# Kernel optimization log

Hardware: AMD Instinct MI355X
Metric: run time of the kernel (lower is better)

## Reference

```python
import jax, jax.numpy as jnp
import numpy as np


def _conv(x, k, pad):
    # x: NHWC, k: HWIO
    return jax.lax.conv_general_dilated(x, k, (1, 1), pad,
                                        dimension_numbers=('NHWC', 'HWIO', 'NHWC'))


def _hard_sigmoid(z):
    return jnp.clip(0.2 * z + 0.5, 0.0, 1.0)


def _convlstm(x_seq, Wx, Wh, b, return_sequences):
    # x_seq: (B,T,H,W,C); Wx: (5,5,C,4F) VALID; Wh: (5,5,F,4F) SAME; b: (4F,)
    B, T, H, W, C = x_seq.shape
    F4 = Wx.shape[-1]
    F = F4 // 4
    # input-to-state convs for all timesteps in one batched conv
    xz = _conv(x_seq.reshape(B * T, H, W, C), Wx, 'VALID') + b
    Ho, Wo = xz.shape[1], xz.shape[2]
    xz = xz.reshape(B, T, Ho, Wo, F4).transpose(1, 0, 2, 3, 4)  # time-major
    h0 = jnp.zeros((B, Ho, Wo, F), x_seq.dtype)
    c0 = h0

    def step(carry, xt):
        h, c = carry
        z = xt + _conv(h, Wh, 'SAME')
        zi, zf, zc, zo = jnp.split(z, 4, axis=-1)  # keras gate order i,f,c,o
        i = _hard_sigmoid(zi)
        f = _hard_sigmoid(zf)
        o = _hard_sigmoid(zo)
        c = f * c + i * jnp.tanh(zc)
        h = o * jnp.tanh(c)
        return (h, c), (h if return_sequences else None)

    (h, c), hs = jax.lax.scan(step, (h0, c0), xz)
    if return_sequences:
        return hs.transpose(1, 0, 2, 3, 4)  # back to (B,T,Ho,Wo,F)
    return h


def setup_inputs() -> dict:
    key = jax.random.key(0)
    ks = jax.random.split(key, 12)
    B, T, H, W, C = 16, 6, 64, 64, 5

    def p(k, shape, scale=0.05):
        return jax.random.normal(k, shape, dtype=jnp.float32) * scale

    x = jax.random.normal(ks[0], (B, T, H, W, C), dtype=jnp.float32)
    # layer1: Cin=5 -> F=128
    Wx1 = p(ks[1], (5, 5, 5, 512));   Wh1 = p(ks[2], (5, 5, 128, 512));  b1 = jnp.zeros((512,), jnp.float32)
    # layer2: Cin=128 -> F=64
    Wx2 = p(ks[3], (5, 5, 128, 256)); Wh2 = p(ks[4], (5, 5, 64, 256));   b2 = jnp.zeros((256,), jnp.float32)
    # layer3: Cin=64 -> F=64
    Wx3 = p(ks[5], (5, 5, 64, 256));  Wh3 = p(ks[6], (5, 5, 64, 256));   b3 = jnp.zeros((256,), jnp.float32)
    D = 52 * 52 * 64  # 173056 after three valid 5x5 convs
    Wd1 = p(ks[7], (D, 1024), 0.01);  bd1 = jnp.zeros((1024,), jnp.float32)
    Wd2 = p(ks[8], (1024, 1024));     bd2 = jnp.zeros((1024,), jnp.float32)
    Wd3 = p(ks[9], (1024, 4));        bd3 = jnp.zeros((4,), jnp.float32)
    return dict(x=x, Wx1=Wx1, Wh1=Wh1, b1=b1, Wx2=Wx2, Wh2=Wh2, b2=b2,
                Wx3=Wx3, Wh3=Wh3, b3=b3, Wd1=Wd1, bd1=bd1, Wd2=Wd2, bd2=bd2,
                Wd3=Wd3, bd3=bd3)


def reference(x, Wx1, Wh1, b1, Wx2, Wh2, b2, Wx3, Wh3, b3,
              Wd1, bd1, Wd2, bd2, Wd3, bd3):
    # NOTE: the original call() computes an average-pool of the input but then
    # overwrites it with conv1(inputs); the pooled branch is dead code.
    h = _convlstm(x, Wx1, Wh1, b1, True)   # (B,T,60,60,128)
    h = _convlstm(h, Wx2, Wh2, b2, True)   # (B,T,56,56,64)
    h = _convlstm(h, Wx3, Wh3, b3, False)  # (B,52,52,64)
    z = h.reshape(h.shape[0], -1)          # keras Flatten = row-major H,W,C
    z = jax.nn.relu(z @ Wd1 + bd1)
    z = jax.nn.relu(z @ Wd2 + bd2)
    return z @ Wd3 + bd3                   # (B,4)
```

## Files before the change

### kernel.cpp

```cpp
#include <hip/hip_runtime.h>

typedef __bf16 bf16;
typedef bf16 bf16x8 __attribute__((ext_vector_type(8)));
typedef float f32x4 __attribute__((ext_vector_type(4)));

__device__ inline bf16x8 bzero8() {
  bf16x8 v;
#pragma unroll
  for (int i = 0; i < 8; ++i) v[i] = (bf16)0.f;
  return v;
}

__device__ __forceinline__ void gload_lds16(const bf16* g, bf16* l) {
  __builtin_amdgcn_global_load_lds(
      (const __attribute__((address_space(1))) void*)g,
      (__attribute__((address_space(3))) void*)l, 16, 0, 0);
}

template <int CIN, int LOG2C>
__global__ void __launch_bounds__(256)
conv_gemm128(const bf16* __restrict__ in, const bf16* __restrict__ wt,
             const float* __restrict__ bias, const bf16* __restrict__ xz,
             bf16* __restrict__ out_bf, float* __restrict__ out_f,
             int HoWo, int Wo, int inH, int inW,
             int T, int t, int N, int K, int epi)
{
  __shared__ bf16 As[128 * 32];
  __shared__ bf16 Bs[128 * 32];

  const int tid  = threadIdx.x;
  const int w    = tid >> 6;
  const int lane = tid & 63;
  const int n0 = blockIdx.x * 128;
  const int m0 = blockIdx.y * 128;

  const int srow = w * 16 + (lane >> 2);
  const int kq   = lane & 3;
  const long inHW = (long)inH * inW;

  long base_a[2];
#pragma unroll
  for (int j = 0; j < 2; ++j) {
    const int am  = m0 + srow + j * 64;
    const int img = am / HoWo;
    const int p   = am - img * HoWo;
    const int ay  = p / Wo;
    const int ax  = p - ay * Wo;
    base_a[j] = (img * inHW + (long)ay * inW + ax) << LOG2C;
  }
  const bf16* wrow0 = wt + (long)(n0 + srow) * K;
  const bf16* wrow1 = wt + (long)(n0 + srow + 64) * K;

  f32x4 acc[4][4];
#pragma unroll
  for (int r = 0; r < 4; ++r)
#pragma unroll
    for (int cq = 0; cq < 4; ++cq) {
      acc[r][cq][0] = 0.f; acc[r][cq][1] = 0.f;
      acc[r][cq][2] = 0.f; acc[r][cq][3] = 0.f;
    }

  const int lrow = lane & 15;
  const int lq   = lane >> 4;
  const int wm   = w & 1;
  const int wn   = w >> 1;
  bf16* AsW = As + w * 512;
  bf16* BsW = Bs + w * 512;

#pragma unroll 4
  for (int k0 = 0; k0 < K; k0 += 32) {
    const int k  = k0 + kq * 8;
    const int c  = k & (CIN - 1);
    const int kc = k >> LOG2C;
    const int ky = kc / 5;
    const int kx = kc - ky * 5;
    const long off = ((long)(ky * inW + kx) << LOG2C) + c;
    gload_lds16(in + base_a[0] + off, AsW);
    gload_lds16(in + base_a[1] + off, AsW + 2048);
    gload_lds16(wrow0 + k, BsW);
    gload_lds16(wrow1 + k, BsW + 2048);
    __syncthreads();

    bf16x8 a_frag[4], b_frag[4];
#pragma unroll
    for (int r = 0; r < 4; ++r)
      a_frag[r] = *(const bf16x8*)&As[(wm * 64 + r * 16 + lrow) * 32 + lq * 8];
#pragma unroll
    for (int cq = 0; cq < 4; ++cq)
      b_frag[cq] = *(const bf16x8*)&Bs[(wn * 64 + cq * 16 + lrow) * 32 + lq * 8];
#pragma unroll
    for (int r = 0; r < 4; ++r)
#pragma unroll
      for (int cq = 0; cq < 4; ++cq)
        acc[r][cq] = __builtin_amdgcn_mfma_f32_16x16x32_bf16(a_frag[r], b_frag[cq],
                                                             acc[r][cq], 0, 0, 0);
    __syncthreads();
  }

  const int colb = n0 + wn * 64 + lrow;
  if (epi == 0) {
    float bsv[4];
#pragma unroll
    for (int cq = 0; cq < 4; ++cq) bsv[cq] = bias[colb + cq * 16];
#pragma unroll
    for (int r = 0; r < 4; ++r)
#pragma unroll
      for (int q = 0; q < 4; ++q) {
        const long row = m0 + wm * 64 + r * 16 + lq * 4 + q;
#pragma unroll
        for (int cq = 0; cq < 4; ++cq)
          out_bf[row * N + colb + cq * 16] = (bf16)(acc[r][cq][q] + bsv[cq]);
      }
  } else {
#pragma unroll
    for (int r = 0; r < 4; ++r)
#pragma unroll
      for (int q = 0; q < 4; ++q) {
        const int row = m0 + wm * 64 + r * 16 + lq * 4 + q;
        const int b   = row / HoWo;
        const int p   = row - b * HoWo;
        const long xrow = (long)(b * T + t) * HoWo + p;
#pragma unroll
        for (int cq = 0; cq < 4; ++cq) {
          const int nn = colb + cq * 16;
          out_f[(long)row * N + nn] = acc[r][cq][q] + (float)xz[xrow * N + nn];
        }
      }
  }
}

template <int CIN>
__global__ void __launch_bounds__(256)
conv_gemm64(const bf16* __restrict__ in, const bf16* __restrict__ wt,
            const float* __restrict__ bias, bf16* __restrict__ out_bf,
            int HoWo, int Wo, int inH, int inW, int N, int K)
{
  __shared__ bf16 As[64 * 40];
  __shared__ bf16 Bs[64 * 40];

  const int tid  = threadIdx.x;
  const int wave = tid >> 6;
  const int lane = tid & 63;
  const int m0 = blockIdx.x * 64;
  const int n0 = blockIdx.y * 64;

  const int srow = tid >> 2;
  const int skq  = tid & 3;

  const int am  = m0 + srow;
  const int ab  = am / HoWo;
  const int apx = am - ab * HoWo;
  const int ay  = apx / Wo;
  const int ax  = apx - ay * Wo;
  const long inHW = (long)inH * inW;
  const bf16* inb  = in + (long)ab * inHW * CIN;
  const bf16* wrow = wt + (long)(n0 + srow) * K;

  f32x4 acc[4];
#pragma unroll
  for (int r = 0; r < 4; ++r) { acc[r][0] = 0.f; acc[r][1] = 0.f; acc[r][2] = 0.f; acc[r][3] = 0.f; }

  const int lrow = lane & 15;
  const int lq   = lane >> 4;
  const int ksteps = (K + 31) >> 5;

  for (int ks = 0; ks < ksteps; ++ks) {
    const int k = (ks << 5) + skq * 8;
    bf16x8 av = bzero8(), bv = bzero8();
#pragma unroll
    for (int j = 0; j < 8; ++j) {
      const int ke = k + j;
      if (ke < K) {
        const int c  = ke % CIN;
        const int kc = ke / CIN;
        const int ky = kc / 5;
        const int kx = kc - ky * 5;
        const int iy = ay + ky;
        const int ix = ax + kx;
        av[j] = inb[((long)iy * inW + ix) * CIN + c];
        bv[j] = wrow[ke];
      }
    }
    *(bf16x8*)&As[srow * 40 + skq * 8] = av;
    *(bf16x8*)&Bs[srow * 40 + skq * 8] = bv;
    __syncthreads();

    bf16x8 bfrag = *(const bf16x8*)&Bs[(wave * 16 + lrow) * 40 + lq * 8];
#pragma unroll
    for (int r = 0; r < 4; ++r) {
      bf16x8 afrag = *(const bf16x8*)&As[(r * 16 + lrow) * 40 + lq * 8];
      acc[r] = __builtin_amdgcn_mfma_f32_16x16x32_bf16(afrag, bfrag, acc[r], 0, 0, 0);
    }
    __syncthreads();
  }

  const int col = n0 + wave * 16 + lrow;
  const float bsv = bias[col];
#pragma unroll
  for (int r = 0; r < 4; ++r)
#pragma unroll
    for (int q = 0; q < 4; ++q) {
      const long row = m0 + r * 16 + lq * 4 + q;
      out_bf[row * N + col] = (bf16)(acc[r][q] + bsv);
    }
}

__global__ void __launch_bounds__(256)
gate_kernel(const bf16* __restrict__ xz, const float* __restrict__ hz,
            float* __restrict__ c, bf16* __restrict__ hseq,
            bf16* __restrict__ hpad, float* __restrict__ hf,
            int HoWo, int Wo, int Wp, int HpWp, int F, int t, int T, int total)
{
  const int idx = blockIdx.x * 256 + threadIdx.x;
  if (idx >= total) return;
  const int f  = idx % F;
  const int bp = idx / F;
  const int b  = bp / HoWo;
  const int p  = bp - b * HoWo;
  const int N4 = 4 * F;

  float zi, zf, zc, zo;
  if (hz != nullptr) {
    const float* zp = hz + (long)bp * N4 + f;
    zi = zp[0]; zf = zp[F]; zc = zp[2 * F]; zo = zp[3 * F];
  } else {
    const bf16* zp = xz + ((long)(b * T + t) * HoWo + p) * N4 + f;
    zi = (float)zp[0]; zf = (float)zp[F]; zc = (float)zp[2 * F]; zo = (float)zp[3 * F];
  }
  const float cprev = (t > 0) ? c[idx] : 0.f;
  const float ig = fminf(fmaxf(0.2f * zi + 0.5f, 0.f), 1.f);
  const float fg = fminf(fmaxf(0.2f * zf + 0.5f, 0.f), 1.f);
  const float og = fminf(fmaxf(0.2f * zo + 0.5f, 0.f), 1.f);
  const float cn = fg * cprev + ig * tanhf(zc);
  const float h  = og * tanhf(cn);
  c[idx] = cn;
  const bf16 hb = (bf16)h;
  if (hseq != nullptr)
    hseq[((long)(b * T + t) * HoWo + p) * F + f] = hb;
  if (hpad != nullptr) {
    const int y = p / Wo;
    const int x = p - y * Wo;
    hpad[((long)b * HpWp + (long)(y + 2) * Wp + (x + 2)) * F + f] = hb;
  }
  if (hf != nullptr) hf[idx] = h;
}

__global__ void __launch_bounds__(256)
cast_f32_bf16(const float* __restrict__ in, bf16* __restrict__ out, int n)
{
  const int i = blockIdx.x * 256 + threadIdx.x;
  if (i < n) out[i] = (bf16)in[i];
}

__global__ void __launch_bounds__(256)
cast_transpose(const float* __restrict__ in, bf16* __restrict__ out, int K, int N)
{
  const int i = blockIdx.x * 256 + threadIdx.x;
  if (i < K * N) {
    const int k = i / N;
    const int n = i - k * N;
    out[(long)n * K + k] = (bf16)in[i];
  }
}

__global__ void __launch_bounds__(256)
dense_splitk(const float* __restrict__ A, const float* __restrict__ W,
             float* __restrict__ out, int D, int N, int chunk)
{
  const int j  = blockIdx.x * 256 + threadIdx.x;
  const int d0 = blockIdx.y * chunk;
  int d1 = d0 + chunk; if (d1 > D) d1 = D;
  float acc[16];
#pragma unroll
  for (int b = 0; b < 16; ++b) acc[b] = 0.f;
  for (int d = d0; d < d1; ++d) {
    const float w = W[(long)d * N + j];
#pragma unroll
    for (int b = 0; b < 16; ++b) acc[b] += A[(long)b * D + d] * w;
  }
#pragma unroll
  for (int b = 0; b < 16; ++b) atomicAdd(&out[b * N + j], acc[b]);
}

__global__ void __launch_bounds__(256)
bias_relu(const float* __restrict__ in, const float* __restrict__ bias,
          float* __restrict__ out, int N, int total)
{
  const int i = blockIdx.x * 256 + threadIdx.x;
  if (i < total) {
    const int j = i % N;
    const float v = in[i] + bias[j];
    out[i] = v > 0.f ? v : 0.f;
  }
}

__global__ void __launch_bounds__(256)
dense3_kernel(const float* __restrict__ z, const float* __restrict__ W,
              const float* __restrict__ bias, float* __restrict__ out)
{
  const int b = blockIdx.x;
  const int tid = threadIdx.x;
  float a0 = 0.f, a1 = 0.f, a2 = 0.f, a3 = 0.f;
  for (int d = tid; d < 1024; d += 256) {
    const float zv = z[b * 1024 + d];
    a0 += zv * W[d * 4 + 0]; a1 += zv * W[d * 4 + 1];
    a2 += zv * W[d * 4 + 2]; a3 += zv * W[d * 4 + 3];
  }
  __shared__ float red[256][4];
  red[tid][0] = a0; red[tid][1] = a1; red[tid][2] = a2; red[tid][3] = a3;
  __syncthreads();
  for (int s = 128; s > 0; s >>= 1) {
    if (tid < s) {
      red[tid][0] += red[tid + s][0]; red[tid][1] += red[tid + s][1];
      red[tid][2] += red[tid + s][2]; red[tid][3] += red[tid + s][3];
    }
    __syncthreads();
  }
  if (tid < 4) out[b * 4 + tid] = red[0][tid] + bias[tid];
}

extern "C" void kernel_launch(void* const* d_in, const int* in_sizes, int n_in,
                              void* d_out, int out_size, void* d_ws, size_t ws_size,
                              hipStream_t stream)
{
  const float* x   = (const float*)d_in[0];
  const float* Wx1 = (const float*)d_in[1];
  const float* Wh1 = (const float*)d_in[2];
  const float* b1  = (const float*)d_in[3];
  const float* Wx2 = (const float*)d_in[4];
  const float* Wh2 = (const float*)d_in[5];
  const float* b2  = (const float*)d_in[6];
  const float* Wx3 = (const float*)d_in[7];
  const float* Wh3 = (const float*)d_in[8];
  const float* b3  = (const float*)d_in[9];
  const float* Wd1 = (const float*)d_in[10];
  const float* bd1 = (const float*)d_in[11];
  const float* Wd2 = (const float*)d_in[12];
  const float* bd2 = (const float*)d_in[13];
  const float* Wd3 = (const float*)d_in[14];
  const float* bd3 = (const float*)d_in[15];

  char* ws = (char*)d_ws;
  size_t off = 0;
  auto alloc = [&](size_t bytes) -> void* {
    void* p = ws + off;
    off += (bytes + 255) & ~(size_t)255;
    return p;
  };
  bf16* x_bf = (bf16*)alloc((size_t)1966080 * 2);
  bf16* wx1t = (bf16*)alloc((size_t)64000 * 2);
  bf16* wh1t = (bf16*)alloc((size_t)1638400 * 2);
  bf16* wx2t = (bf16*)alloc((size_t)819200 * 2);
  bf16* wh2t = (bf16*)alloc((size_t)409600 * 2);
  bf16* wx3t = (bf16*)alloc((size_t)409600 * 2);
  bf16* wh3t = (bf16*)alloc((size_t)409600 * 2);
  bf16* xzA  = (bf16*)alloc((size_t)176947200 * 2);
  bf16* hB   = (bf16*)alloc((size_t)44236800 * 2);
  float* hzC = (float*)alloc((size_t)29491200 * 4);
  float* cA  = (float*)alloc((size_t)7372800 * 4);
  float* h3f = (float*)alloc((size_t)2768896 * 4);
  bf16* hpadA = (bf16*)alloc((size_t)8388608 * 2);
  float* out1 = (float*)alloc(16384 * 4);
  float* z1   = (float*)alloc(16384 * 4);
  float* out2 = (float*)alloc(16384 * 4);
  float* z2   = (float*)alloc(16384 * 4);

  bf16* h1seq = hB;
  bf16* h2seq = hB;
  float* c1 = cA;
  float* c2 = cA;
  float* c3 = cA + (size_t)3211264;
  bf16* hpad1 = hpadA;
  bf16* hpad2 = hpadA;
  bf16* hpad3 = hpadA + (size_t)3686400;

  cast_f32_bf16<<<(1966080 + 255) / 256, 256, 0, stream>>>(x, x_bf, 1966080);
  cast_transpose<<<(64000 + 255) / 256, 256, 0, stream>>>(Wx1, wx1t, 125, 512);
  cast_transpose<<<(1638400 + 255) / 256, 256, 0, stream>>>(Wh1, wh1t, 3200, 512);
  cast_transpose<<<(819200 + 255) / 256, 256, 0, stream>>>(Wx2, wx2t, 3200, 256);
  cast_transpose<<<(409600 + 255) / 256, 256, 0, stream>>>(Wh2, wh2t, 1600, 256);
  cast_transpose<<<(409600 + 255) / 256, 256, 0, stream>>>(Wx3, wx3t, 1600, 256);
  cast_transpose<<<(409600 + 255) / 256, 256, 0, stream>>>(Wh3, wh3t, 1600, 256);

  hipMemsetAsync(hpadA, 0, (size_t)8388608 * 2, stream);
  conv_gemm64<5><<<dim3(5400, 8), 256, 0, stream>>>(
      x_bf, wx1t, b1, xzA, 3600, 60, 64, 64, 512, 125);
  for (int t = 0; t < 6; ++t) {
    if (t > 0)
      conv_gemm128<128, 7><<<dim3(4, 450), 256, 0, stream>>>(
          hpad1, wh1t, nullptr, xzA, nullptr, hzC,
          3600, 60, 64, 64, 6, t, 512, 3200, 1);
    gate_kernel<<<28800, 256, 0, stream>>>(
        xzA, (t > 0) ? hzC : nullptr, c1, h1seq,
        (t < 5) ? hpad1 : nullptr, nullptr,
        3600, 60, 64, 4096, 128, t, 6, 7372800);
  }

  bf16* xz2 = xzA;
  conv_gemm128<128, 7><<<dim3(2, 2352), 256, 0, stream>>>(
      h1seq, wx2t, b2, nullptr, xz2, nullptr,
      3136, 56, 60, 60, 6, 0, 256, 3200, 0);
  hipMemsetAsync(hpad2, 0, (size_t)3686400 * 2, stream);
  for (int t = 0; t < 6; ++t) {
    if (t > 0)
      conv_gemm128<64, 6><<<dim3(2, 392), 256, 0, stream>>>(
          hpad2, wh2t, nullptr, xz2, nullptr, hzC,
          3136, 56, 60, 60, 6, t, 256, 1600, 1);
    gate_kernel<<<12544, 256, 0, stream>>>(
        xz2, (t > 0) ? hzC : nullptr, c2, h2seq,
        (t < 5) ? hpad2 : nullptr, nullptr,
        3136, 56, 60, 3600, 64, t, 6, 3211264);
  }

  bf16* xz3 = xzA;
  conv_gemm128<64, 6><<<dim3(2, 2028), 256, 0, stream>>>(
      h2seq, wx3t, b3, nullptr, xz3, nullptr,
      2704, 52, 56, 56, 6, 0, 256, 1600, 0);
  hipMemsetAsync(hpad3, 0, (size_t)3211264 * 2, stream);
  for (int t = 0; t < 6; ++t) {
    if (t > 0)
      conv_gemm128<64, 6><<<dim3(2, 338), 256, 0, stream>>>(
          hpad3, wh3t, nullptr, xz3, nullptr, hzC,
          2704, 52, 56, 56, 6, t, 256, 1600, 1);
    gate_kernel<<<10816, 256, 0, stream>>>(
        xz3, (t > 0) ? hzC : nullptr, c3, nullptr,
        (t < 5) ? hpad3 : nullptr, (t == 5) ? h3f : nullptr,
        2704, 52, 56, 3136, 64, t, 6, 2768896);
  }

  hipMemsetAsync(out1, 0, 16384 * 4, stream);
  hipMemsetAsync(out2, 0, 16384 * 4, stream);
  dense_splitk<<<dim3(4, 169), 256, 0, stream>>>(h3f, Wd1, out1, 173056, 1024, 1024);
  bias_relu<<<64, 256, 0, stream>>>(out1, bd1, z1, 1024, 16384);
  dense_splitk<<<dim3(4, 4), 256, 0, stream>>>(z1, Wd2, out2, 1024, 1024, 256);
  bias_relu<<<64, 256, 0, stream>>>(out2, bd2, z2, 1024, 16384);
  dense3_kernel<<<16, 256, 0, stream>>>(z2, Wd3, bd3, (float*)d_out);
}
```

Baseline: 5.428 ms.

## Rewrite implicit-GEMM conv as 256x256 double-buffered pipelined MFMA kernel

Replaces the 128x128 single-buffered conv GEMM with a 256x256-tile, 512-thread kernel that uses K=64 steps. It double-buffers LDS and interleaves async global-to-LDS loads for the next tile with MFMA quadrants, using raw barriers, vmcnt waits and setprio. It also XOR-swizzles the LDS layout to avoid bank conflicts and remaps workgroups across XCDs for L2 locality. The aim is to hide load latency and raise arithmetic intensity. The cost is higher register and LDS use, and fewer blocks for the small recurrent convs (e.g. 169-225 blocks), which may underfill the GPU.

```diff
diff --git a/kernel.cpp b/kernel.cpp
--- a/kernel.cpp
+++ b/kernel.cpp
@@ -17,113 +17,220 @@
       (__attribute__((address_space(3))) void*)l, 16, 0, 0);
 }
 
+#define MFMA16 __builtin_amdgcn_mfma_f32_16x16x32_bf16
+#define LGKM0 asm volatile("s_waitcnt lgkmcnt(0)")
+#define VMC2 asm volatile("s_waitcnt vmcnt(2)")
+#define VMC0 asm volatile("s_waitcnt vmcnt(0)")
+
 template <int CIN, int LOG2C>
-__global__ void __launch_bounds__(256)
-conv_gemm128(const bf16* __restrict__ in, const bf16* __restrict__ wt,
+__global__ void __launch_bounds__(512, 2)
+conv_gemm256(const bf16* __restrict__ in, const bf16* __restrict__ wt,
              const float* __restrict__ bias, const bf16* __restrict__ xz,
              bf16* __restrict__ out_bf, float* __restrict__ out_f,
              int HoWo, int Wo, int inH, int inW,
              int T, int t, int N, int K, int epi)
 {
-  __shared__ bf16 As[128 * 32];
-  __shared__ bf16 Bs[128 * 32];
+  __shared__ bf16 As[2][2][8192];
+  __shared__ bf16 Bs[2][2][8192];
 
   const int tid  = threadIdx.x;
   const int w    = tid >> 6;
   const int lane = tid & 63;
-  const int n0 = blockIdx.x * 128;
-  const int m0 = blockIdx.y * 128;
-
-  const int srow = w * 16 + (lane >> 2);
-  const int kq   = lane & 3;
+
+  const int gx  = gridDim.x;
+  const int nwg = gx * gridDim.y;
+  int flat = blockIdx.y * gx + blockIdx.x;
+  {
+    const int xcd = flat & 7, o = flat >> 3;
+    const int qq = nwg >> 3, rr = nwg & 7;
+    flat = (xcd < rr ? xcd * (qq + 1) : rr * (qq + 1) + (xcd - rr) * qq) + o;
+  }
+  const int n0 = (flat % gx) << 8;
+  const int m0 = (flat / gx) << 8;
+
   const long inHW = (long)inH * inW;
-
-  long base_a[2];
-#pragma unroll
-  for (int j = 0; j < 2; ++j) {
-    const int am  = m0 + srow + j * 64;
-    const int img = am / HoWo;
-    const int p   = am - img * HoWo;
-    const int ay  = p / Wo;
-    const int ax  = p - ay * Wo;
-    base_a[j] = (img * inHW + (long)ay * inW + ax) << LOG2C;
-  }
-  const bf16* wrow0 = wt + (long)(n0 + srow) * K;
-  const bf16* wrow1 = wt + (long)(n0 + srow + 64) * K;
-
-  f32x4 acc[4][4];
-#pragma unroll
-  for (int r = 0; r < 4; ++r)
-#pragma unroll
-    for (int cq = 0; cq < 4; ++cq) {
-      acc[r][cq][0] = 0.f; acc[r][cq][1] = 0.f;
-      acc[r][cq][2] = 0.f; acc[r][cq][3] = 0.f;
-    }
+  const int lr8  = lane >> 3;
+  const int koff = ((lane & 7) ^ lr8) << 3;
+
+  long baseA[2][2];
+  const bf16* wrowp[2][2];
+#pragma unroll
+  for (int h = 0; h < 2; ++h)
+#pragma unroll
+    for (int j = 0; j < 2; ++j) {
+      const int row = ((j * 8 + w) << 3) + lr8;
+      const int gm  = m0 + h * 128 + row;
+      const int img = gm / HoWo;
+      const int p   = gm - img * HoWo;
+      const int ay  = p / Wo;
+      const int ax  = p - ay * Wo;
+      baseA[h][j] = ((long)img * inHW + (long)ay * inW + ax) << LOG2C;
+      wrowp[h][j] = wt + (long)(n0 + h * 128 + row) * K + koff;
+    }
+
+  const int KT = K >> 6;
+
+  auto stage = [&](int kt, int half) {
+    if (kt >= KT) return;
+    const int slot = kt & 1;
+    if (half < 2) {
+      const int kk = kt << 6;
+      const int kc = kk >> LOG2C;
+      const int ky = kc / 5;
+      const int kx = kc - ky * 5;
+      const long toff = ((long)(ky * inW + kx) << LOG2C) + (kk & (CIN - 1)) + koff;
+      bf16* d = &As[slot][half][w << 9];
+      gload_lds16(in + baseA[half][0] + toff, d);
+      gload_lds16(in + baseA[half][1] + toff, d + 4096);
+    } else {
+      const int h = half - 2;
+      bf16* d = &Bs[slot][h][w << 9];
+      gload_lds16(wrowp[h][0] + (kt << 6), d);
+      gload_lds16(wrowp[h][1] + (kt << 6), d + 4096);
+    }
+  };
 
   const int lrow = lane & 15;
   const int lq   = lane >> 4;
-  const int wm   = w & 1;
-  const int wn   = w >> 1;
-  bf16* AsW = As + w * 512;
-  bf16* BsW = Bs + w * 512;
-
-#pragma unroll 4
-  for (int k0 = 0; k0 < K; k0 += 32) {
-    const int k  = k0 + kq * 8;
-    const int c  = k & (CIN - 1);
-    const int kc = k >> LOG2C;
-    const int ky = kc / 5;
-    const int kx = kc - ky * 5;
-    const long off = ((long)(ky * inW + kx) << LOG2C) + c;
-    gload_lds16(in + base_a[0] + off, AsW);
-    gload_lds16(in + base_a[1] + off, AsW + 2048);
-    gload_lds16(wrow0 + k, BsW);
-    gload_lds16(wrow1 + k, BsW + 2048);
-    __syncthreads();
-
-    bf16x8 a_frag[4], b_frag[4];
-#pragma unroll
-    for (int r = 0; r < 4; ++r)
-      a_frag[r] = *(const bf16x8*)&As[(wm * 64 + r * 16 + lrow) * 32 + lq * 8];
-#pragma unroll
-    for (int cq = 0; cq < 4; ++cq)
-      b_frag[cq] = *(const bf16x8*)&Bs[(wn * 64 + cq * 16 + lrow) * 32 + lq * 8];
-#pragma unroll
-    for (int r = 0; r < 4; ++r)
-#pragma unroll
-      for (int cq = 0; cq < 4; ++cq)
-        acc[r][cq] = __builtin_amdgcn_mfma_f32_16x16x32_bf16(a_frag[r], b_frag[cq],
-                                                             acc[r][cq], 0, 0, 0);
-    __syncthreads();
-  }
+  const int wm   = w >> 2;
+  const int wn   = w & 3;
+  const int s7   = lrow & 7;
+
+  auto rdA = [&](int slot, int r, int ks) -> bf16x8 {
+    const int row = (r << 4) + lrow;
+    const int ch  = ((ks << 2) + lq) ^ s7;
+    return *(const bf16x8*)&As[slot][wm][(row << 6) + (ch << 3)];
+  };
+  auto rdB = [&](int slot, int cq, int ks) -> bf16x8 {
+    const int row = ((wn & 1) << 6) + (cq << 4) + lrow;
+    const int ch  = ((ks << 2) + lq) ^ s7;
+    return *(const bf16x8*)&Bs[slot][wn >> 1][(row << 6) + (ch << 3)];
+  };
+
+  f32x4 acc[8][4];
+#pragma unroll
+  for (int r = 0; r < 8; ++r)
+#pragma unroll
+    for (int c = 0; c < 4; ++c) {
+      acc[r][c][0] = 0.f; acc[r][c][1] = 0.f;
+      acc[r][c][2] = 0.f; acc[r][c][3] = 0.f;
+    }
+
+#define QUAD(RB, CB)                                                          \
+  __builtin_amdgcn_s_setprio(1);                                              \
+  _Pragma("unroll")                                                           \
+  for (int r = 0; r < 4; ++r)                                                 \
+    _Pragma("unroll")                                                         \
+    for (int c = 0; c < 2; ++c) {                                             \
+      acc[RB + r][CB + c] =                                                   \
+          MFMA16(af[r][0], bq[CB + c][0], acc[RB + r][CB + c], 0, 0, 0);      \
+      acc[RB + r][CB + c] =                                                   \
+          MFMA16(af[r][1], bq[CB + c][1], acc[RB + r][CB + c], 0, 0, 0);      \
+    }                                                                         \
+  __builtin_amdgcn_s_setprio(0);
+
+  stage(0, 0); stage(0, 1); stage(0, 2); stage(0, 3);
+  stage(1, 0);
+  VMC2;
+  __builtin_amdgcn_s_barrier();
+
+  bf16x8 af[4][2], bq[4][2];
+  const int NI = KT >> 1;
+  for (int i = 0; i < NI; ++i) {
+    const int t1 = 2 * i + 1, t2 = 2 * i + 2, t3 = 2 * i + 3;
+#pragma unroll
+    for (int r = 0; r < 4; ++r) { af[r][0] = rdA(0, r, 0); af[r][1] = rdA(0, r, 1); }
+#pragma unroll
+    for (int c = 0; c < 2; ++c) { bq[c][0] = rdB(0, c, 0); bq[c][1] = rdB(0, c, 1); }
+    stage(t1, 1);
+    __builtin_amdgcn_s_barrier(); LGKM0;
+    QUAD(0, 0)
+    __builtin_amdgcn_s_barrier();
+#pragma unroll
+    for (int c = 2; c < 4; ++c) { bq[c][0] = rdB(0, c, 0); bq[c][1] = rdB(0, c, 1); }
+    stage(t1, 2);
+    __builtin_amdgcn_s_barrier(); LGKM0;
+    QUAD(0, 2)
+    __builtin_amdgcn_s_barrier();
+#pragma unroll
+    for (int r = 0; r < 4; ++r) { af[r][0] = rdA(0, r + 4, 0); af[r][1] = rdA(0, r + 4, 1); }
+    stage(t1, 3);
+    __builtin_amdgcn_s_barrier(); LGKM0;
+    QUAD(4, 2)
+    __builtin_amdgcn_s_barrier();
+    stage(t2, 0);
+    __builtin_amdgcn_s_barrier(); LGKM0;
+    QUAD(4, 0)
+    if (t2 < KT) { VMC2; } else { VMC0; }
+    __builtin_amdgcn_s_barrier();
+#pragma unroll
+    for (int r = 0; r < 4; ++r) { af[r][0] = rdA(1, r, 0); af[r][1] = rdA(1, r, 1); }
+#pragma unroll
+    for (int c = 0; c < 2; ++c) { bq[c][0] = rdB(1, c, 0); bq[c][1] = rdB(1, c, 1); }
+    stage(t2, 1);
+    __builtin_amdgcn_s_barrier(); LGKM0;
+    QUAD(0, 0)
+    __builtin_amdgcn_s_barrier();
+#pragma unroll
+    for (int c = 2; c < 4; ++c) { bq[c][0] = rdB(1, c, 0); bq[c][1] = rdB(1, c, 1); }
+    stage(t2, 2);
+    __builtin_amdgcn_s_barrier(); LGKM0;
+    QUAD(0, 2)
+    __builtin_amdgcn_s_barrier();
+#pragma unroll
+    for (int r = 0; r < 4; ++r) { af[r][0] = rdA(1, r + 4, 0); af[r][1] = rdA(1, r + 4, 1); }
+    stage(t2, 3);
+    __builtin_amdgcn_s_barrier(); LGKM0;
+    QUAD(4, 2)
+    __builtin_amdgcn_s_barrier();
+    stage(t3, 0);
+    __builtin_amdgcn_s_barrier(); LGKM0;
+    QUAD(4, 0)
+    if (t3 < KT) { VMC2; } else { VMC0; }
+    __builtin_amdgcn_s_barrier();
+  }
+
+  if (KT & 1) {
+#pragma unroll
+    for (int r = 0; r < 4; ++r) { af[r][0] = rdA(0, r, 0); af[r][1] = rdA(0, r, 1); }
+#pragma unroll
+    for (int c = 0; c < 4; ++c) { bq[c][0] = rdB(0, c, 0); bq[c][1] = rdB(0, c, 1); }
+    QUAD(0, 0)
+    QUAD(0, 2)
+#pragma unroll
+    for (int r = 0; r < 4; ++r) { af[r][0] = rdA(0, r + 4, 0); af[r][1] = rdA(0, r + 4, 1); }
+    QUAD(4, 0)
+    QUAD(4, 2)
+  }
+#undef QUAD
 
   const int colb = n0 + wn * 64 + lrow;
   if (epi == 0) {
     float bsv[4];
 #pragma unroll
-    for (int cq = 0; cq < 4; ++cq) bsv[cq] = bias[colb + cq * 16];
-#pragma unroll
-    for (int r = 0; r < 4; ++r)
+    for (int c = 0; c < 4; ++c) bsv[c] = bias[colb + c * 16];
+#pragma unroll
+    for (int r = 0; r < 8; ++r)
 #pragma unroll
       for (int q = 0; q < 4; ++q) {
-        const long row = m0 + wm * 64 + r * 16 + lq * 4 + q;
-#pragma unroll
-        for (int cq = 0; cq < 4; ++cq)
-          out_bf[row * N + colb + cq * 16] = (bf16)(acc[r][cq][q] + bsv[cq]);
+        const long row = m0 + wm * 128 + r * 16 + lq * 4 + q;
+#pragma unroll
+        for (int c = 0; c < 4; ++c)
+          out_bf[row * N + colb + c * 16] = (bf16)(acc[r][c][q] + bsv[c]);
       }
   } else {
 #pragma unroll
-    for (int r = 0; r < 4; ++r)
+    for (int r = 0; r < 8; ++r)
 #pragma unroll
       for (int q = 0; q < 4; ++q) {
-        const int row = m0 + wm * 64 + r * 16 + lq * 4 + q;
+        const int row = m0 + wm * 128 + r * 16 + lq * 4 + q;
         const int b   = row / HoWo;
         const int p   = row - b * HoWo;
         const long xrow = (long)(b * T + t) * HoWo + p;
 #pragma unroll
-        for (int cq = 0; cq < 4; ++cq) {
-          const int nn = colb + cq * 16;
-          out_f[(long)row * N + nn] = acc[r][cq][q] + (float)xz[xrow * N + nn];
+        for (int c = 0; c < 4; ++c) {
+          const int nn = colb + c * 16;
+          out_f[(long)row * N + nn] = acc[r][c][q] + (float)xz[xrow * N + nn];
         }
       }
   }
@@ -189,7 +296,7 @@
 #pragma unroll
     for (int r = 0; r < 4; ++r) {
       bf16x8 afrag = *(const bf16x8*)&As[(r * 16 + lrow) * 40 + lq * 8];
-      acc[r] = __builtin_amdgcn_mfma_f32_16x16x32_bf16(afrag, bfrag, acc[r], 0, 0, 0);
+      acc[r] = MFMA16(afrag, bfrag, acc[r], 0, 0, 0);
     }
     __syncthreads();
   }
@@ -387,7 +494,7 @@
       x_bf, wx1t, b1, xzA, 3600, 60, 64, 64, 512, 125);
   for (int t = 0; t < 6; ++t) {
     if (t > 0)
-      conv_gemm128<128, 7><<<dim3(4, 450), 256, 0, stream>>>(
+      conv_gemm256<128, 7><<<dim3(2, 225), 512, 0, stream>>>(
           hpad1, wh1t, nullptr, xzA, nullptr, hzC,
           3600, 60, 64, 64, 6, t, 512, 3200, 1);
     gate_kernel<<<28800, 256, 0, stream>>>(
@@ -397,13 +504,13 @@
   }
 
   bf16* xz2 = xzA;
-  conv_gemm128<128, 7><<<dim3(2, 2352), 256, 0, stream>>>(
+  conv_gemm256<128, 7><<<dim3(1, 1176), 512, 0, stream>>>(
       h1seq, wx2t, b2, nullptr, xz2, nullptr,
       3136, 56, 60, 60, 6, 0, 256, 3200, 0);
   hipMemsetAsync(hpad2, 0, (size_t)3686400 * 2, stream);
   for (int t = 0; t < 6; ++t) {
     if (t > 0)
-      conv_gemm128<64, 6><<<dim3(2, 392), 256, 0, stream>>>(
+      conv_gemm256<64, 6><<<dim3(1, 196), 512, 0, stream>>>(
           hpad2, wh2t, nullptr, xz2, nullptr, hzC,
           3136, 56, 60, 60, 6, t, 256, 1600, 1);
     gate_kernel<<<12544, 256, 0, stream>>>(
@@ -413,13 +520,13 @@
   }
 
   bf16* xz3 = xzA;
-  conv_gemm128<64, 6><<<dim3(2, 2028), 256, 0, stream>>>(
+  conv_gemm256<64, 6><<<dim3(1, 1014), 512, 0, stream>>>(
       h2seq, wx3t, b3, nullptr, xz3, nullptr,
       2704, 52, 56, 56, 6, 0, 256, 1600, 0);
   hipMemsetAsync(hpad3, 0, (size_t)3211264 * 2, stream);
   for (int t = 0; t < 6; ++t) {
     if (t > 0)
-      conv_gemm128<64, 6><<<dim3(2, 338), 256, 0, stream>>>(
+      conv_gemm256<64, 6><<<dim3(1, 169), 512, 0, stream>>>(
           hpad3, wh3t, nullptr, xz3, nullptr, hzC,
           2704, 52, 56, 56, 6, t, 256, 1600, 1);
     gate_kernel<<<10816, 256, 0, stream>>>(
```

After: 4.687 ms. 1.16x faster.
